# Optimization experiments

Measured on AMD Instinct MI355X. Metric: run time of the kernel, lower is better.

## Reference

```python
import jax, jax.numpy as jnp
import numpy as np

ALPHA = 0.2
MOMENTUM = 0.8
M = 430   # int(256 * 1.68)
D = 512


def l2norm(x, axis=-1, eps=1e-12):
    # matches torch F.normalize(dim=-1)
    n = jnp.linalg.norm(x, axis=axis, keepdims=True)
    return x / jnp.maximum(n, eps)


def setup_inputs() -> dict:
    key = jax.random.key(0)
    k1, k2, k3, k4, k5, k6 = jax.random.split(key, 6)
    text_token = jax.random.normal(k1, (768, D), dtype=jnp.float32)
    image_token4 = jax.random.normal(k2, (16, 4096, D), dtype=jnp.float32)
    image_token8 = jax.random.normal(k3, (16, 1024, D), dtype=jnp.float32)
    image_token12 = jax.random.normal(k4, (16, 256, D), dtype=jnp.float32)
    # memory cache initialized like F.normalize(torch.rand(m, d))
    cache = l2norm(jax.random.uniform(k5, (M, D), dtype=jnp.float32))
    # extractor: Linear(2d -> d, bias=False); torch weight shape [d, 2d]
    W = jax.random.normal(k6, (D, 2 * D), dtype=jnp.float32) * (1.0 / np.sqrt(2 * D))
    return {"text_token": text_token, "image_token4": image_token4,
            "image_token8": image_token8, "image_token12": image_token12,
            "cache": cache, "W": W}


def _write_one(img, cache):
    """One scale of write(): top-1 routed, column-max-normalized scatter-reduce."""
    d = cache.shape[1]
    base = l2norm(img.reshape(-1, d))                 # [N, d]
    score = base @ cache.T                            # [N, M]
    sq = jax.nn.softmax(score, axis=0)                # softmax over queries
    top1 = jnp.argmax(score, axis=1)                  # top-1 of softmax == argmax of score
    colmax = jnp.max(sq, axis=0)                      # [M]  max over ALL queries per slot
    n = base.shape[0]
    w = sq[jnp.arange(n), top1] / colmax[top1]        # [N] per-query weight
    sums = jax.ops.segment_sum(w[:, None] * base, top1, num_segments=M)   # [M, d]
    cnt = jax.ops.segment_sum(jnp.ones((n,), base.dtype), top1, num_segments=M)
    upd = jnp.where(cnt[:, None] > 0,
                    MOMENTUM * cache + (1.0 - MOMENTUM) * sums,
                    cache)
    return l2norm(upd)


def reference(text_token, image_token4, image_token8, image_token12, cache, W):
    # ---- read ----
    base = l2norm(text_token)                         # [C, d]
    score = base @ cache.T                            # [C, M]
    fine = jax.nn.softmax(score, axis=1) @ cache      # [C, d]
    # ---- extractor + residual ----
    text_fine = ALPHA * (jnp.concatenate([text_token, fine], axis=-1) @ W.T) + text_token
    # ---- write (training): three scales, all against the same original cache ----
    new_cache = (_write_one(image_token4, cache)
                 + _write_one(image_token8, cache)
                 + _write_one(image_token12, cache)) / 3.0
    # ---- training loss ----
    loss = jnp.mean(jnp.abs(l2norm(text_fine) - text_token))
    return text_fine, loss, new_cache
```

## Files before the change

### kernel.cpp

```cpp
#include <hip/hip_runtime.h>
#include <math.h>

#define TC 768
#define DD 512
#define MM 430
#define MP 448
#define WNT 14
#define N0 65536
#define N1 16384
#define N2 4096
#define OFF1 65536
#define OFF2 81920
#define NTOT 86016
constexpr float kALPHA = 0.2f;
constexpr float kMOM   = 0.8f;

typedef short bf16x8 __attribute__((ext_vector_type(8)));
typedef float f32x4 __attribute__((ext_vector_type(4)));

__device__ __forceinline__ size_t fragidx(int tile, int col, int k, int K) {
  return (size_t)tile * 16 * K + ((((k >> 5) * 64 + ((k >> 3) & 3) * 16 + col)) << 3) + (k & 7);
}

__device__ __forceinline__ float wave_reduce_sum(float v) {
#pragma unroll
  for (int o = 32; o > 0; o >>= 1) v += __shfl_down(v, o);
  return v;
}
__device__ __forceinline__ float wave_reduce_max(float v) {
#pragma unroll
  for (int o = 32; o > 0; o >>= 1) v = fmaxf(v, __shfl_down(v, o));
  return v;
}
__device__ __forceinline__ unsigned int fkey(float f) {
  unsigned int b = __float_as_uint(f);
  return (b & 0x80000000u) ? ~b : (b | 0x80000000u);
}
__device__ __forceinline__ float fdecode(unsigned int k) {
  return __uint_as_float((k & 0x80000000u) ? (k & 0x7FFFFFFFu) : ~k);
}
__device__ __forceinline__ unsigned short f2bf(float f) {
  unsigned int u = __float_as_uint(f);
  u += 0x7FFFu + ((u >> 16) & 1u);
  return (unsigned short)(u >> 16);
}
__device__ __forceinline__ float bf2f(unsigned short u) {
  return __uint_as_float(((unsigned int)u) << 16);
}
__device__ __forceinline__ void gload_lds16(const unsigned short* g, unsigned short* l) {
  __builtin_amdgcn_global_load_lds(
      (const __attribute__((address_space(1))) void*)g,
      (__attribute__((address_space(3))) void*)l, 16, 0, 0);
}

__global__ __launch_bounds__(256) void k_prep(
    const float* __restrict__ text, const float* __restrict__ W,
    const float* __restrict__ cache,
    unsigned short* __restrict__ tb, float* __restrict__ invT,
    unsigned short* __restrict__ wb,
    unsigned short* __restrict__ cb, unsigned short* __restrict__ cbT,
    float* __restrict__ sums, float* __restrict__ outnc,
    int* __restrict__ cnt, unsigned int* __restrict__ colkey,
    float* __restrict__ out_loss) {
  const int b = blockIdx.x, tid = threadIdx.x;
  if (b < 768) {
    __shared__ float sred[8];
    const int c = b, lane = tid & 63, wid = tid >> 6;
    float x0 = text[(size_t)c * DD + tid];
    float x1 = text[(size_t)c * DD + 256 + tid];
    float ss = x0 * x0 + x1 * x1;
    ss = wave_reduce_sum(ss);
    if (lane == 0) sred[wid] = ss;
    __syncthreads();
    if (tid == 0) {
      float t = sred[0] + sred[1] + sred[2] + sred[3];
      invT[c] = 1.0f / fmaxf(sqrtf(t), 1e-12f);
    }
    const int rtile = c >> 4, colc = c & 15;
    tb[fragidx(rtile, colc, tid, DD)] = f2bf(x0);
    tb[fragidx(rtile, colc, tid + 256, DD)] = f2bf(x1);
  } else if (b < 1280) {
    const int j = b - 768;
    const int jt = j >> 4, colc = j & 15;
    float4 v = *(const float4*)(W + (size_t)j * 1024 + tid * 4);
    const float vv[4] = {v.x, v.y, v.z, v.w};
#pragma unroll
    for (int e = 0; e < 4; e++)
      wb[fragidx(jt, colc, tid * 4 + e, 1024)] = f2bf(vv[e]);
  } else if (b < 1728) {
    const int m = b - 1280;
    const int mt16 = m >> 4, colm = m & 15;
    for (int d = tid; d < DD; d += 256) {
      unsigned short v = (m < MM) ? f2bf(cache[(size_t)m * DD + d]) : (unsigned short)0;
      cb[fragidx(mt16, colm, d, DD)] = v;
      cbT[fragidx(d >> 4, d & 15, m, MP)] = v;
    }
  } else {
    const int ib = b - 1728;
    const int idx = ib * 1024 + tid * 4;
    float4 z = make_float4(0.f, 0.f, 0.f, 0.f);
    if (idx < 3 * MM * DD) *(float4*)(sums + idx) = z;
    else *(float4*)(outnc + (idx - 3 * MM * DD)) = z;
    if (ib == 0) {
#pragma unroll
      for (int i = 0; i < 6; i++) {
        cnt[tid + i * 256] = 0;
        colkey[tid + i * 256] = 0u;
      }
      if (tid == 0) out_loss[0] = 0.f;
    }
  }
}

__global__ __launch_bounds__(512, 2) void k_score_plus(
    const float* __restrict__ img4, const float* __restrict__ img8,
    const float* __restrict__ img12, const unsigned short* __restrict__ cb,
    int* __restrict__ top1, float* __restrict__ topval,
    float* __restrict__ invn, unsigned int* __restrict__ colkey,
    int* __restrict__ cnt,
    const unsigned short* __restrict__ tb, const float* __restrict__ invT,
    unsigned short* __restrict__ pb) {
  __shared__ __align__(16) unsigned char smem[2 * 32 * DD * 2 + MP * 4];
  const int b = blockIdx.x;
  const int tid = threadIdx.x;
  const int lane = tid & 63;
  const int col = lane & 15, grp = lane >> 4;

  if (b < 672) {
    unsigned short* ldsB = (unsigned short*)smem;
    unsigned int* scol = (unsigned int*)(smem + 2 * 32 * DD * 2);
    const float* img;
    int n0, off, sc;
    if (b < 512)      { sc = 0; img = img4;  n0 = b * 128;         off = 0; }
    else if (b < 640) { sc = 1; img = img8;  n0 = (b - 512) * 128; off = OFF1; }
    else              { sc = 2; img = img12; n0 = (b - 640) * 128; off = OFF2; }
    const int w = tid >> 6;
    const int nw = n0 + w * 16;

    for (int i = tid; i < MP; i += 512) scol[i] = 0u;

#pragma unroll
    for (int i = 0; i < 4; i++)
      gload_lds16(cb + (i * 512 + tid) * 8, ldsB + (i * 512 + tid) * 8);

    bf16x8 afrag[16];
    float ss = 0.f;
    {
      const float* arow = img + (size_t)(nw + col) * DD + grp * 8;
#pragma unroll
      for (int kk = 0; kk < 16; kk++) {
        float4 f0 = *(const float4*)(arow + kk * 32);
        float4 f1 = *(const float4*)(arow + kk * 32 + 4);
        ss += f0.x * f0.x + f0.y * f0.y + f0.z * f0.z + f0.w * f0.w +
              f1.x * f1.x + f1.y * f1.y + f1.z * f1.z + f1.w * f1.w;
        bf16x8 a;
        a[0] = (short)f2bf(f0.x); a[1] = (short)f2bf(f0.y);
        a[2] = (short)f2bf(f0.z); a[3] = (short)f2bf(f0.w);
        a[4] = (short)f2bf(f1.x); a[5] = (short)f2bf(f1.y);
        a[6] = (short)f2bf(f1.z); a[7] = (short)f2bf(f1.w);
        afrag[kk] = a;
      }
    }
    ss += __shfl_xor(ss, 16);
    ss += __shfl_xor(ss, 32);
    const float inv = 1.0f / fmaxf(sqrtf(ss), 1e-12f);
    if (grp == 0) invn[off + nw + col] = inv;
    float invr[4];
#pragma unroll
    for (int i = 0; i < 4; i++) invr[i] = __shfl(inv, grp * 4 + i);

    float bestv[4];
    int besti[4];
#pragma unroll
    for (int i = 0; i < 4; i++) { bestv[i] = -1e30f; besti[i] = 0; }

    __syncthreads();

    for (int mt = 0; mt < WNT; mt++) {
      const int cur = mt & 1;
      if (mt + 1 < WNT) {
        const unsigned short* src = cb + (size_t)(mt + 1) * (32 * DD);
        unsigned short* dst = ldsB + (cur ^ 1) * (32 * DD);
#pragma unroll
        for (int i = 0; i < 4; i++)
          gload_lds16(src + (i * 512 + tid) * 8, dst + (i * 512 + tid) * 8);
      }
      f32x4 acc[2][2];
#pragma unroll
      for (int c = 0; c < 2; c++)
#pragma unroll
        for (int e = 0; e < 2; e++) acc[c][e] = (f32x4){0.f, 0.f, 0.f, 0.f};
      const unsigned short* lb = ldsB + cur * (32 * DD);
#pragma unroll
      for (int kk = 0; kk < 16; kk++) {
        bf16x8 b0 = *(const bf16x8*)(lb + ((0 * 16 + kk) * 64 + lane) * 8);
        bf16x8 b1 = *(const bf16x8*)(lb + ((1 * 16 + kk) * 64 + lane) * 8);
        const int eo = kk & 1;
        acc[0][eo] = __builtin_amdgcn_mfma_f32_16x16x32_bf16(afrag[kk], b0, acc[0][eo], 0, 0, 0);
        acc[1][eo] = __builtin_amdgcn_mfma_f32_16x16x32_bf16(afrag[kk], b1, acc[1][eo], 0, 0, 0);
      }
#pragma unroll
      for (int c = 0; c < 2; c++) {
        const int gcol = mt * 32 + c * 16 + col;
        float colm = -1e30f;
#pragma unroll
        for (int i = 0; i < 4; i++) {
          float v = (acc[c][0][i] + acc[c][1][i]) * invr[i];
          colm = fmaxf(colm, v);
          if (gcol < MM && v > bestv[i]) { bestv[i] = v; besti[i] = gcol; }
        }
        colm = fmaxf(colm, __shfl_xor(colm, 16));
        colm = fmaxf(colm, __shfl_xor(colm, 32));
        if (grp == 0 && gcol < MM) atomicMax(&scol[gcol], fkey(colm));
      }
      __syncthreads();
    }

#pragma unroll
    for (int i = 0; i < 4; i++) {
      float v = bestv[i];
      int idx = besti[i];
#pragma unroll
      for (int mask = 1; mask < 16; mask <<= 1) {
        float ov = __shfl_xor(v, mask);
        int oi = __shfl_xor(idx, mask);
        if (ov > v || (ov == v && oi < idx)) { v = ov; idx = oi; }
      }
      if (col == 0) {
        const int row = nw + grp * 4 + i;
        top1[off + row] = idx;
        topval[off + row] = v;
        atomicAdd(cnt + sc * 512 + idx, 1);
      }
    }
    __syncthreads();
    for (int i = tid; i < MM; i += 512) atomicMax(&colkey[sc * 512 + i], scol[i]);
  } else {
    const int h = tid >> 8;
    const int wh = (tid >> 6) & 3;
    const int rtile = (b - 672) * 2 + h;
    const int rowbase = rtile * 16;
    unsigned short (*sc16)[MP] = (unsigned short(*)[MP])smem + h * 16;

    bf16x8 afrag[16];
#pragma unroll
    for (int kk = 0; kk < 16; kk++)
      afrag[kk] = *(const bf16x8*)(tb + (size_t)rtile * 8192 + (kk * 64 + lane) * 8);
    float invv = invT[rowbase + col];
    float invr[4];
#pragma unroll
    for (int i = 0; i < 4; i++) invr[i] = __shfl(invv, grp * 4 + i);

    for (int j = 0; j < 7; j++) {
      const int mt = wh * 7 + j;
      const unsigned short* bbase = cb + (size_t)mt * 8192;
      f32x4 a0 = {0.f, 0.f, 0.f, 0.f}, a1 = {0.f, 0.f, 0.f, 0.f};
#pragma unroll
      for (int kk = 0; kk < 16; kk += 2) {
        bf16x8 b0 = *(const bf16x8*)(bbase + (kk * 64 + lane) * 8);
        bf16x8 b1 = *(const bf16x8*)(bbase + ((kk + 1) * 64 + lane) * 8);
        a0 = __builtin_amdgcn_mfma_f32_16x16x32_bf16(afrag[kk], b0, a0, 0, 0, 0);
        a1 = __builtin_amdgcn_mfma_f32_16x16x32_bf16(afrag[kk + 1], b1, a1, 0, 0, 0);
      }
      const int gcol = mt * 16 + col;
#pragma unroll
      for (int i = 0; i < 4; i++)
        sc16[grp * 4 + i][gcol] = f2bf((a0[i] + a1[i]) * invr[i]);
    }
    __syncthreads();

    for (int r0 = 0; r0 < 4; r0++) {
      const int rl = wh * 4 + r0;
      const unsigned short* srow = &sc16[rl][0];
      float mx = -1e30f;
      for (int m = lane; m < MM; m += 64) mx = fmaxf(mx, bf2f(srow[m]));
      mx = wave_reduce_max(mx);
      mx = __shfl(mx, 0);
      float sum = 0.f;
      for (int m = lane; m < MM; m += 64) sum += __expf(bf2f(srow[m]) - mx);
      sum = wave_reduce_sum(sum);
      sum = __shfl(sum, 0);
      const float invZ = 1.0f / sum;
      for (int m = lane; m < MP; m += 64) {
        float p = (m < MM) ? __expf(bf2f(srow[m]) - mx) * invZ : 0.f;
        pb[fragidx(rtile, rl, m, MP)] = f2bf(p);
      }
    }
  }
}

__global__ __launch_bounds__(512) void k_prefix(
    const int* __restrict__ cnt, int* __restrict__ woffs) {
  __shared__ int s[512];
  const int sc = blockIdx.x, t = threadIdx.x;
  const int c = (t < MM) ? cnt[sc * 512 + t] : 0;
  s[t] = c;
  __syncthreads();
#pragma unroll
  for (int d = 1; d < 512; d <<= 1) {
    int v = (t >= d) ? s[t - d] : 0;
    __syncthreads();
    s[t] += v;
    __syncthreads();
  }
  if (t < MM) woffs[sc * 512 + t] = s[t] - c;
}

__global__ __launch_bounds__(256) void k_pv_sort(
    const int* __restrict__ top1, int* __restrict__ woffs,
    int* __restrict__ sorted,
    const unsigned short* __restrict__ pb, const unsigned short* __restrict__ cbT,
    unsigned short* __restrict__ fb) {
  const int b = blockIdx.x, tid = threadIdx.x;
  if (b < 336) {
    int sc, loc, off;
    if (b < 256)      { sc = 0; loc = b;        off = 0; }
    else if (b < 320) { sc = 1; loc = b - 256;  off = OFF1; }
    else              { sc = 2; loc = b - 320;  off = OFF2; }
    const int n = loc * 256 + tid;
    const int slot = top1[off + n];
    const int pos = atomicAdd(&woffs[sc * 512 + slot], 1);
    sorted[off + pos] = n;
  } else {
    const int fp = b - 336;
    const int bx = fp % 12, by = fp / 12;
    const int w = tid >> 6, lane = tid & 63;
    const int col = lane & 15, grp = lane >> 4;
    const int rowbase = bx * 64 + w * 16;
    const int rtile = rowbase >> 4;
    const int dt0 = by * 8;
    bf16x8 afrag[14];
#pragma unroll
    for (int kk = 0; kk < 14; kk++)
      afrag[kk] = *(const bf16x8*)(pb + (size_t)rtile * 7168 + (kk * 64 + lane) * 8);
    for (int dt = dt0; dt < dt0 + 8; dt++) {
      f32x4 a0 = {0.f, 0.f, 0.f, 0.f}, a1 = {0.f, 0.f, 0.f, 0.f};
#pragma unroll
      for (int kk = 0; kk < 14; kk += 2) {
        bf16x8 b0 = *(const bf16x8*)(cbT + (size_t)dt * 7168 + (kk * 64 + lane) * 8);
        bf16x8 b1 = *(const bf16x8*)(cbT + (size_t)dt * 7168 + ((kk + 1) * 64 + lane) * 8);
        a0 = __builtin_amdgcn_mfma_f32_16x16x32_bf16(afrag[kk], b0, a0, 0, 0, 0);
        a1 = __builtin_amdgcn_mfma_f32_16x16x32_bf16(afrag[kk + 1], b1, a1, 0, 0, 0);
      }
#pragma unroll
      for (int i = 0; i < 4; i++) {
        const int d = dt * 16 + col;
        fb[fragidx(rtile, grp * 4 + i, d, DD)] = f2bf(a0[i] + a1[i]);
      }
    }
  }
}

__global__ __launch_bounds__(256) void k_ext_accum(
    const float* __restrict__ img4, const float* __restrict__ img8,
    const float* __restrict__ img12, const float* __restrict__ invn,
    const int* __restrict__ top1, const float* __restrict__ topval,
    const unsigned int* __restrict__ colkey, const int* __restrict__ sorted,
    float* __restrict__ sums,
    const unsigned short* __restrict__ tb, const unsigned short* __restrict__ fb,
    const unsigned short* __restrict__ wb, const float* __restrict__ text,
    float* __restrict__ out) {
  __shared__ int s_n[128];
  __shared__ int s_slot[128];
  __shared__ float s_w[128];
  const int b = blockIdx.x, tid = threadIdx.x;
  if (b < 672) {
    const float* img;
    int r0, off, sc;
    if (b < 512)      { sc = 0; img = img4;  r0 = b * 128;         off = 0; }
    else if (b < 640) { sc = 1; img = img8;  r0 = (b - 512) * 128; off = OFF1; }
    else              { sc = 2; img = img12; r0 = (b - 640) * 128; off = OFF2; }
    float* sums_s = sums + (size_t)sc * MM * DD;
    if (tid < 128) {
      int n = sorted[off + r0 + tid];
      int sl = top1[off + n];
      s_n[tid] = n;
      s_slot[tid] = sl;
      s_w[tid] = __expf(topval[off + n] - fdecode(colkey[sc * 512 + sl])) * invn[off + n];
    }
    __syncthreads();
    float ax = 0.f, ay = 0.f;
    int cur = s_slot[0];
    for (int r = 0; r < 128; r++) {
      int sl = s_slot[r];
      if (sl != cur) {
        atomicAdd(&sums_s[(size_t)cur * DD + tid * 2], ax);
        atomicAdd(&sums_s[(size_t)cur * DD + tid * 2 + 1], ay);
        ax = 0.f; ay = 0.f; cur = sl;
      }
      const float2 v = *(const float2*)(img + (size_t)s_n[r] * DD + tid * 2);
      const float w = s_w[r];
      ax += w * v.x;
      ay += w * v.y;
    }
    atomicAdd(&sums_s[(size_t)cur * DD + tid * 2], ax);
    atomicAdd(&sums_s[(size_t)cur * DD + tid * 2 + 1], ay);
  } else {
    const int ea = b - 672;
    const int bx = ea % 12, by = ea / 12;
    const int w = tid >> 6, lane = tid & 63;
    const int col = lane & 15, grp = lane >> 4;
    const int rowbase = bx * 64 + w * 16;
    const int rtile = rowbase >> 4;
    const int jt0 = by * 8;
    bf16x8 afrag[32];
#pragma unroll
    for (int kk = 0; kk < 16; kk++)
      afrag[kk] = *(const bf16x8*)(tb + (size_t)rtile * 8192 + (kk * 64 + lane) * 8);
#pragma unroll
    for (int kk = 0; kk < 16; kk++)
      afrag[16 + kk] = *(const bf16x8*)(fb + (size_t)rtile * 8192 + (kk * 64 + lane) * 8);
    for (int jt = jt0; jt < jt0 + 8; jt++) {
      f32x4 a0 = {0.f, 0.f, 0.f, 0.f}, a1 = {0.f, 0.f, 0.f, 0.f};
#pragma unroll
      for (int kk = 0; kk < 32; kk += 2) {
        bf16x8 b0 = *(const bf16x8*)(wb + (size_t)jt * 16384 + (kk * 64 + lane) * 8);
        bf16x8 b1 = *(const bf16x8*)(wb + (size_t)jt * 16384 + ((kk + 1) * 64 + lane) * 8);
        a0 = __builtin_amdgcn_mfma_f32_16x16x32_bf16(afrag[kk], b0, a0, 0, 0, 0);
        a1 = __builtin_amdgcn_mfma_f32_16x16x32_bf16(afrag[kk + 1], b1, a1, 0, 0, 0);
      }
#pragma unroll
      for (int i = 0; i < 4; i++) {
        const int row = rowbase + grp * 4 + i;
        const int j = jt * 16 + col;
        out[(size_t)row * DD + j] = kALPHA * (a0[i] + a1[i]) + text[(size_t)row * DD + j];
      }
    }
  }
}

__global__ __launch_bounds__(256) void k_upd_loss(
    const float* __restrict__ cache, const float* __restrict__ sums,
    const int* __restrict__ cnt, float* __restrict__ outnc,
    const float* __restrict__ out, const float* __restrict__ text,
    float* __restrict__ out_loss) {
  __shared__ float sred[8];
  const int b = blockIdx.x, tid = threadIdx.x, lane = tid & 63, wid = tid >> 6;
  if (b < 3 * MM) {
    const int sc = b / MM, m = b % MM;
    const float* sums_s = sums + (size_t)sc * MM * DD;
    float c0 = cache[(size_t)m * DD + tid], c1 = cache[(size_t)m * DD + 256 + tid];
    float u0, u1;
    if (cnt[sc * 512 + m] > 0) {
      u0 = kMOM * c0 + (1.0f - kMOM) * sums_s[(size_t)m * DD + tid];
      u1 = kMOM * c1 + (1.0f - kMOM) * sums_s[(size_t)m * DD + 256 + tid];
    } else {
      u0 = c0; u1 = c1;
    }
    float ss = u0 * u0 + u1 * u1;
    ss = wave_reduce_sum(ss);
    if (lane == 0) sred[wid] = ss;
    __syncthreads();
    if (tid == 0) sred[0] = sred[0] + sred[1] + sred[2] + sred[3];
    __syncthreads();
    const float inv3 = (1.0f / 3.0f) / fmaxf(sqrtf(sred[0]), 1e-12f);
    atomicAdd(&outnc[(size_t)m * DD + tid], u0 * inv3);
    atomicAdd(&outnc[(size_t)m * DD + 256 + tid], u1 * inv3);
  } else {
    const int c = b - 3 * MM;
    float t0 = out[(size_t)c * DD + tid], t1 = out[(size_t)c * DD + 256 + tid];
    float ss = t0 * t0 + t1 * t1;
    ss = wave_reduce_sum(ss);
    if (lane == 0) sred[wid] = ss;
    __syncthreads();
    if (tid == 0) sred[0] = sred[0] + sred[1] + sred[2] + sred[3];
    __syncthreads();
    float inv = 1.0f / fmaxf(sqrtf(sred[0]), 1e-12f);
    float s = fabsf(t0 * inv - text[(size_t)c * DD + tid]) +
              fabsf(t1 * inv - text[(size_t)c * DD + 256 + tid]);
    s = wave_reduce_sum(s);
    __syncthreads();
    if (lane == 0) sred[wid] = s;
    __syncthreads();
    if (tid == 0)
      atomicAdd(out_loss, (sred[0] + sred[1] + sred[2] + sred[3]) / (float)(TC * DD));
  }
}

extern "C" void kernel_launch(void* const* d_in, const int* in_sizes, int n_in,
                              void* d_out, int out_size, void* d_ws, size_t ws_size,
                              hipStream_t stream) {
  const float* text  = (const float*)d_in[0];
  const float* img4  = (const float*)d_in[1];
  const float* img8  = (const float*)d_in[2];
  const float* img12 = (const float*)d_in[3];
  const float* cache = (const float*)d_in[4];
  const float* W     = (const float*)d_in[5];
  float* out = (float*)d_out;
  float* out_loss = out + (size_t)TC * DD;
  float* out_nc   = out + (size_t)TC * DD + 1;

  char* p = (char*)d_ws;
  float* invn          = (float*)p; p += NTOT * sizeof(float);
  int* top1            = (int*)p;   p += NTOT * sizeof(int);
  float* topval        = (float*)p; p += NTOT * sizeof(float);
  int* sorted          = (int*)p;   p += NTOT * sizeof(int);
  unsigned int* colkey = (unsigned int*)p; p += 3 * 512 * sizeof(unsigned int);
  float* sums          = (float*)p; p += (size_t)3 * MM * DD * sizeof(float);
  int* cnt             = (int*)p;   p += 3 * 512 * sizeof(int);
  int* woffs           = (int*)p;   p += 3 * 512 * sizeof(int);
  unsigned short* cb   = (unsigned short*)p; p += (size_t)MP * DD * sizeof(unsigned short);
  unsigned short* cbT  = (unsigned short*)p; p += (size_t)DD * MP * sizeof(unsigned short);
  unsigned short* tb   = (unsigned short*)p; p += (size_t)TC * DD * sizeof(unsigned short);
  unsigned short* pb   = (unsigned short*)p; p += (size_t)TC * MP * sizeof(unsigned short);
  unsigned short* fb   = (unsigned short*)p; p += (size_t)TC * DD * sizeof(unsigned short);
  unsigned short* wb   = (unsigned short*)p; p += (size_t)DD * 1024 * sizeof(unsigned short);
  float* invT          = (float*)p; p += 1024 * sizeof(float);
  (void)in_sizes; (void)n_in; (void)out_size; (void)ws_size;

  k_prep<<<dim3(2588), dim3(256), 0, stream>>>(text, W, cache, tb, invT, wb,
                                               cb, cbT, sums, out_nc, cnt, colkey,
                                               out_loss);
  k_score_plus<<<dim3(696), dim3(512), 0, stream>>>(img4, img8, img12, cb,
                                                    top1, topval, invn, colkey, cnt,
                                                    tb, invT, pb);
  k_prefix<<<dim3(3), dim3(512), 0, stream>>>(cnt, woffs);
  k_pv_sort<<<dim3(384), dim3(256), 0, stream>>>(top1, woffs, sorted, pb, cbT, fb);
  k_ext_accum<<<dim3(720), dim3(256), 0, stream>>>(img4, img8, img12, invn,
                                                   top1, topval, colkey, sorted, sums,
                                                   tb, fb, wb, text, out);
  k_upd_loss<<<dim3(2058), dim3(256), 0, stream>>>(cache, sums, cnt, out_nc,
                                                   out, text, out_loss);
}
```

Measured before the change: 226.8 us.

## Switch image scoring to 32x32x16 MFMA with packed argmax keys

The image-vs-cache scoring GEMM now uses 32x32x16 bf16 MFMA tiles. Each wave covers 32 rows and each block covers 256 rows, so the block count is halved. A new 32-wide fragment layout of the cache is produced in prep for this. The argmax packs the value's sortable key with the inverted column index into one uint, which replaces the float/int pair shuffles. The exchange is higher register pressure (32 A fragments plus 16-wide accumulators), the removal of the occupancy-2 launch bound, and slightly truncated top values because the key keeps only the high bits.

```diff
diff --git a/kernel.cpp b/kernel.cpp
--- a/kernel.cpp
+++ b/kernel.cpp
@@ -5,7 +5,7 @@
 #define DD 512
 #define MM 430
 #define MP 448
-#define WNT 14
+#define WNT32 14
 #define N0 65536
 #define N1 16384
 #define N2 4096
@@ -17,9 +17,13 @@
 
 typedef short bf16x8 __attribute__((ext_vector_type(8)));
 typedef float f32x4 __attribute__((ext_vector_type(4)));
+typedef float f32x16 __attribute__((ext_vector_type(16)));
 
 __device__ __forceinline__ size_t fragidx(int tile, int col, int k, int K) {
   return (size_t)tile * 16 * K + ((((k >> 5) * 64 + ((k >> 3) & 3) * 16 + col)) << 3) + (k & 7);
+}
+__device__ __forceinline__ size_t fragidx32(int tile, int s, int k) {
+  return (size_t)tile * 16384 + ((((k >> 4) * 64) + ((k >> 3) & 1) * 32 + s) << 3) + (k & 7);
 }
 
 __device__ __forceinline__ float wave_reduce_sum(float v) {
@@ -59,6 +63,7 @@
     unsigned short* __restrict__ tb, float* __restrict__ invT,
     unsigned short* __restrict__ wb,
     unsigned short* __restrict__ cb, unsigned short* __restrict__ cbT,
+    unsigned short* __restrict__ cb32,
     float* __restrict__ sums, float* __restrict__ outnc,
     int* __restrict__ cnt, unsigned int* __restrict__ colkey,
     float* __restrict__ out_loss) {
@@ -90,10 +95,12 @@
   } else if (b < 1728) {
     const int m = b - 1280;
     const int mt16 = m >> 4, colm = m & 15;
+    const int t32 = m >> 5, s32 = m & 31;
     for (int d = tid; d < DD; d += 256) {
       unsigned short v = (m < MM) ? f2bf(cache[(size_t)m * DD + d]) : (unsigned short)0;
       cb[fragidx(mt16, colm, d, DD)] = v;
       cbT[fragidx(d >> 4, d & 15, m, MP)] = v;
+      cb32[fragidx32(t32, s32, d)] = v;
     }
   } else {
     const int ib = b - 1728;
@@ -112,45 +119,46 @@
   }
 }
 
-__global__ __launch_bounds__(512, 2) void k_score_plus(
+__global__ __launch_bounds__(512) void k_score_plus(
     const float* __restrict__ img4, const float* __restrict__ img8,
-    const float* __restrict__ img12, const unsigned short* __restrict__ cb,
+    const float* __restrict__ img12, const unsigned short* __restrict__ cb32,
+    const unsigned short* __restrict__ cb,
     int* __restrict__ top1, float* __restrict__ topval,
     float* __restrict__ invn, unsigned int* __restrict__ colkey,
     int* __restrict__ cnt,
     const unsigned short* __restrict__ tb, const float* __restrict__ invT,
     unsigned short* __restrict__ pb) {
-  __shared__ __align__(16) unsigned char smem[2 * 32 * DD * 2 + MP * 4];
+  __shared__ __align__(16) unsigned char smem[2 * 16384 * 2 + MP * 4];
   const int b = blockIdx.x;
   const int tid = threadIdx.x;
   const int lane = tid & 63;
-  const int col = lane & 15, grp = lane >> 4;
-
-  if (b < 672) {
+
+  if (b < 336) {
     unsigned short* ldsB = (unsigned short*)smem;
-    unsigned int* scol = (unsigned int*)(smem + 2 * 32 * DD * 2);
+    unsigned int* scol = (unsigned int*)(smem + 2 * 16384 * 2);
     const float* img;
     int n0, off, sc;
-    if (b < 512)      { sc = 0; img = img4;  n0 = b * 128;         off = 0; }
-    else if (b < 640) { sc = 1; img = img8;  n0 = (b - 512) * 128; off = OFF1; }
-    else              { sc = 2; img = img12; n0 = (b - 640) * 128; off = OFF2; }
+    if (b < 256)      { sc = 0; img = img4;  n0 = b * 256;         off = 0; }
+    else if (b < 320) { sc = 1; img = img8;  n0 = (b - 256) * 256; off = OFF1; }
+    else              { sc = 2; img = img12; n0 = (b - 320) * 256; off = OFF2; }
     const int w = tid >> 6;
-    const int nw = n0 + w * 16;
+    const int r32 = lane & 31, hi = lane >> 5;
+    const int nw = n0 + w * 32;
 
     for (int i = tid; i < MP; i += 512) scol[i] = 0u;
 
 #pragma unroll
     for (int i = 0; i < 4; i++)
-      gload_lds16(cb + (i * 512 + tid) * 8, ldsB + (i * 512 + tid) * 8);
-
-    bf16x8 afrag[16];
+      gload_lds16(cb32 + (i * 512 + tid) * 8, ldsB + (i * 512 + tid) * 8);
+
+    bf16x8 afrag[32];
     float ss = 0.f;
     {
-      const float* arow = img + (size_t)(nw + col) * DD + grp * 8;
-#pragma unroll
-      for (int kk = 0; kk < 16; kk++) {
-        float4 f0 = *(const float4*)(arow + kk * 32);
-        float4 f1 = *(const float4*)(arow + kk * 32 + 4);
+      const float* arow = img + (size_t)(nw + r32) * DD + hi * 8;
+#pragma unroll
+      for (int kk = 0; kk < 32; kk++) {
+        float4 f0 = *(const float4*)(arow + kk * 16);
+        float4 f1 = *(const float4*)(arow + kk * 16 + 4);
         ss += f0.x * f0.x + f0.y * f0.y + f0.z * f0.z + f0.w * f0.w +
               f1.x * f1.x + f1.y * f1.y + f1.z * f1.z + f1.w * f1.w;
         bf16x8 a;
@@ -161,84 +169,76 @@
         afrag[kk] = a;
       }
     }
-    ss += __shfl_xor(ss, 16);
     ss += __shfl_xor(ss, 32);
     const float inv = 1.0f / fmaxf(sqrtf(ss), 1e-12f);
-    if (grp == 0) invn[off + nw + col] = inv;
-    float invr[4];
-#pragma unroll
-    for (int i = 0; i < 4; i++) invr[i] = __shfl(inv, grp * 4 + i);
-
-    float bestv[4];
-    int besti[4];
-#pragma unroll
-    for (int i = 0; i < 4; i++) { bestv[i] = -1e30f; besti[i] = 0; }
-
-    __syncthreads();
-
-    for (int mt = 0; mt < WNT; mt++) {
+    if (lane < 32) invn[off + nw + r32] = inv;
+    float invr16[16];
+#pragma unroll
+    for (int r = 0; r < 16; r++)
+      invr16[r] = __shfl(inv, (r & 3) + 8 * (r >> 2) + 4 * hi);
+
+    unsigned int bestkey[16];
+#pragma unroll
+    for (int r = 0; r < 16; r++) bestkey[r] = 0u;
+
+    __syncthreads();
+
+    for (int mt = 0; mt < WNT32; mt++) {
       const int cur = mt & 1;
-      if (mt + 1 < WNT) {
-        const unsigned short* src = cb + (size_t)(mt + 1) * (32 * DD);
-        unsigned short* dst = ldsB + (cur ^ 1) * (32 * DD);
+      if (mt + 1 < WNT32) {
+        const unsigned short* src = cb32 + (size_t)(mt + 1) * 16384;
+        unsigned short* dst = ldsB + (cur ^ 1) * 16384;
 #pragma unroll
         for (int i = 0; i < 4; i++)
           gload_lds16(src + (i * 512 + tid) * 8, dst + (i * 512 + tid) * 8);
       }
-      f32x4 acc[2][2];
-#pragma unroll
-      for (int c = 0; c < 2; c++)
-#pragma unroll
-        for (int e = 0; e < 2; e++) acc[c][e] = (f32x4){0.f, 0.f, 0.f, 0.f};
-      const unsigned short* lb = ldsB + cur * (32 * DD);
-#pragma unroll
-      for (int kk = 0; kk < 16; kk++) {
-        bf16x8 b0 = *(const bf16x8*)(lb + ((0 * 16 + kk) * 64 + lane) * 8);
-        bf16x8 b1 = *(const bf16x8*)(lb + ((1 * 16 + kk) * 64 + lane) * 8);
-        const int eo = kk & 1;
-        acc[0][eo] = __builtin_amdgcn_mfma_f32_16x16x32_bf16(afrag[kk], b0, acc[0][eo], 0, 0, 0);
-        acc[1][eo] = __builtin_amdgcn_mfma_f32_16x16x32_bf16(afrag[kk], b1, acc[1][eo], 0, 0, 0);
-      }
-#pragma unroll
-      for (int c = 0; c < 2; c++) {
-        const int gcol = mt * 32 + c * 16 + col;
-        float colm = -1e30f;
-#pragma unroll
-        for (int i = 0; i < 4; i++) {
-          float v = (acc[c][0][i] + acc[c][1][i]) * invr[i];
-          colm = fmaxf(colm, v);
-          if (gcol < MM && v > bestv[i]) { bestv[i] = v; besti[i] = gcol; }
+      f32x16 acc0 = {}, acc1 = {};
+      const unsigned short* lb = ldsB + cur * 16384;
+#pragma unroll
+      for (int kk = 0; kk < 32; kk += 2) {
+        bf16x8 b0 = *(const bf16x8*)(lb + (kk * 64 + lane) * 8);
+        bf16x8 b1 = *(const bf16x8*)(lb + ((kk + 1) * 64 + lane) * 8);
+        acc0 = __builtin_amdgcn_mfma_f32_32x32x16_bf16(afrag[kk], b0, acc0, 0, 0, 0);
+        acc1 = __builtin_amdgcn_mfma_f32_32x32x16_bf16(afrag[kk + 1], b1, acc1, 0, 0, 0);
+      }
+      const int gcol = mt * 32 + r32;
+      const bool valid = (gcol < MM);
+      float colm = -1e30f;
+#pragma unroll
+      for (int r = 0; r < 16; r++) {
+        float v = (acc0[r] + acc1[r]) * invr16[r];
+        colm = fmaxf(colm, v);
+        if (valid) {
+          unsigned int key = (fkey(v) & ~511u) | (unsigned int)(511 - gcol);
+          bestkey[r] = max(bestkey[r], key);
         }
-        colm = fmaxf(colm, __shfl_xor(colm, 16));
-        colm = fmaxf(colm, __shfl_xor(colm, 32));
-        if (grp == 0 && gcol < MM) atomicMax(&scol[gcol], fkey(colm));
-      }
+      }
+      colm = fmaxf(colm, __shfl_xor(colm, 32));
+      if (lane < 32 && valid) atomicMax(&scol[gcol], fkey(colm));
       __syncthreads();
     }
 
 #pragma unroll
-    for (int i = 0; i < 4; i++) {
-      float v = bestv[i];
-      int idx = besti[i];
-#pragma unroll
-      for (int mask = 1; mask < 16; mask <<= 1) {
-        float ov = __shfl_xor(v, mask);
-        int oi = __shfl_xor(idx, mask);
-        if (ov > v || (ov == v && oi < idx)) { v = ov; idx = oi; }
-      }
-      if (col == 0) {
-        const int row = nw + grp * 4 + i;
-        top1[off + row] = idx;
-        topval[off + row] = v;
-        atomicAdd(cnt + sc * 512 + idx, 1);
+    for (int r = 0; r < 16; r++) {
+      unsigned int key = bestkey[r];
+#pragma unroll
+      for (int mask = 1; mask < 32; mask <<= 1)
+        key = max(key, __shfl_xor(key, mask));
+      if (r32 == 0) {
+        const int row = nw + (r & 3) + 8 * (r >> 2) + 4 * hi;
+        const int gcol = 511 - (int)(key & 511u);
+        top1[off + row] = gcol;
+        topval[off + row] = fdecode(key & ~511u);
+        atomicAdd(cnt + sc * 512 + gcol, 1);
       }
     }
     __syncthreads();
     for (int i = tid; i < MM; i += 512) atomicMax(&colkey[sc * 512 + i], scol[i]);
   } else {
+    const int col = lane & 15, grp = lane >> 4;
     const int h = tid >> 8;
     const int wh = (tid >> 6) & 3;
-    const int rtile = (b - 672) * 2 + h;
+    const int rtile = (b - 336) * 2 + h;
     const int rowbase = rtile * 16;
     unsigned short (*sc16)[MP] = (unsigned short(*)[MP])smem + h * 16;
 
@@ -501,6 +501,7 @@
   int* woffs           = (int*)p;   p += 3 * 512 * sizeof(int);
   unsigned short* cb   = (unsigned short*)p; p += (size_t)MP * DD * sizeof(unsigned short);
   unsigned short* cbT  = (unsigned short*)p; p += (size_t)DD * MP * sizeof(unsigned short);
+  unsigned short* cb32 = (unsigned short*)p; p += (size_t)MP * DD * sizeof(unsigned short);
   unsigned short* tb   = (unsigned short*)p; p += (size_t)TC * DD * sizeof(unsigned short);
   unsigned short* pb   = (unsigned short*)p; p += (size_t)TC * MP * sizeof(unsigned short);
   unsigned short* fb   = (unsigned short*)p; p += (size_t)TC * DD * sizeof(unsigned short);
@@ -509,9 +510,9 @@
   (void)in_sizes; (void)n_in; (void)out_size; (void)ws_size;
 
   k_prep<<<dim3(2588), dim3(256), 0, stream>>>(text, W, cache, tb, invT, wb,
-                                               cb, cbT, sums, out_nc, cnt, colkey,
-                                               out_loss);
-  k_score_plus<<<dim3(696), dim3(512), 0, stream>>>(img4, img8, img12, cb,
+                                               cb, cbT, cb32, sums, out_nc, cnt,
+                                               colkey, out_loss);
+  k_score_plus<<<dim3(360), dim3(512), 0, stream>>>(img4, img8, img12, cb32, cb,
                                                     top1, topval, invn, colkey, cnt,
                                                     tb, invT, pb);
   k_prefix<<<dim3(3), dim3(512), 0, stream>>>(cnt, woffs);
```

New measurement: 285.8 us. 26.0% more time.
